# Kernel tuning notes

Hardware: AMD Instinct MI355X
Metric: run time of the kernel (lower is better)

Reference implementation:

```python
import jax, jax.numpy as jnp
import numpy as np

B, T, D_FEAT, FREQ, HID = 256, 128, 128, 16, 128


def setup_inputs() -> dict:
    key = jax.random.key(0)
    ks = jax.random.split(key, 14)
    n = lambda k, s, sc: jax.random.normal(k, s, jnp.float32) * sc
    sx = float(np.sqrt(2.0 / (D_FEAT + HID)))   # xavier-ish for W_*
    sf = float(np.sqrt(2.0 / (D_FEAT + FREQ)))
    sh = float(np.sqrt(1.0 / HID))              # stand-in for orthogonal U_*
    return {
        "input": jax.random.normal(ks[0], (B, D_FEAT * T), jnp.float32),
        "W_i": n(ks[1], (D_FEAT, HID), sx), "U_i": n(ks[2], (HID, HID), sh), "b_i": jnp.zeros((HID,), jnp.float32),
        "W_ste": n(ks[3], (D_FEAT, HID), sx), "U_ste": n(ks[4], (HID, HID), sh), "b_ste": jnp.ones((HID,), jnp.float32),
        "W_fre": n(ks[5], (D_FEAT, FREQ), sf), "U_fre": n(ks[6], (HID, FREQ), sh), "b_fre": jnp.ones((FREQ,), jnp.float32),
        "W_c": n(ks[7], (D_FEAT, HID), sx), "U_c": n(ks[8], (HID, HID), sh), "b_c": jnp.zeros((HID,), jnp.float32),
        "W_o": n(ks[9], (D_FEAT, HID), sx), "U_o": n(ks[10], (HID, HID), sh), "b_o": jnp.zeros((HID,), jnp.float32),
        "U_a": n(ks[11], (FREQ, 1), sh), "b_a": jnp.zeros((HID,), jnp.float32),
        "W_sym": n(ks[12], (HID, 1), sh), "b_sym": jnp.zeros((1,), jnp.float32),
    }


def _hsig(z):  # torch.nn.Hardsigmoid: relu6(x+3)/6
    return jnp.clip(z / 6.0 + 0.5, 0.0, 1.0)


def reference(input, W_i, U_i, b_i, W_ste, U_ste, b_ste, W_fre, U_fre, b_fre,
              W_c, U_c, b_c, W_o, U_o, b_o, U_a, b_a, W_sym, b_sym):
    Bsz = input.shape[0]
    x = input.reshape(Bsz, D_FEAT, -1).transpose(0, 2, 1)  # (B, T, D)
    # hoist the 5 input projections out of the time loop (identical math)
    xi = jnp.einsum('btd,dh->tbh', x, W_i) + b_i
    xste = jnp.einsum('btd,dh->tbh', x, W_ste) + b_ste
    xfre = jnp.einsum('btd,df->tbf', x, W_fre) + b_fre
    xc = jnp.einsum('btd,dh->tbh', x, W_c) + b_c
    xo = jnp.einsum('btd,dh->tbh', x, W_o) + b_o
    frequency = jnp.arange(FREQ, dtype=jnp.float32) / FREQ
    two_pi = jnp.float32(2.0 * np.pi)
    ua = U_a[:, 0]  # (FREQ,)

    def step(carry, xs):
        h, S_re, S_im, t = carry
        xi_t, xste_t, xfre_t, xc_t, xo_t = xs
        i = _hsig(xi_t + h @ U_i)
        ste = _hsig(xste_t + h @ U_ste)
        fre = _hsig(xfre_t + h @ U_fre)
        f = ste[:, :, None] * fre[:, None, :]          # (B, H, F)
        c = i * jnp.tanh(xc_t + h @ U_c)               # (B, H)
        t = t + 1.0
        omega = two_pi * t * frequency                 # (F,)
        S_re = f * S_re + c[:, :, None] * jnp.cos(omega)
        S_im = f * S_im + c[:, :, None] * jnp.sin(omega)
        A = S_re * S_re + S_im * S_im                  # (B, H, F)
        a = jnp.tanh(jnp.einsum('bhf,f->bh', A, ua) + b_a)
        o = _hsig(xo_t + h @ U_o)
        h = o * a
        return (h, S_re, S_im, t), None

    init = (jnp.zeros((Bsz, HID), jnp.float32),
            jnp.zeros((Bsz, HID, FREQ), jnp.float32),
            jnp.zeros((Bsz, HID, FREQ), jnp.float32),
            jnp.float32(0.0))
    (h, _, _, _), _ = jax.lax.scan(step, init, (xi, xste, xfre, xc, xo))
    return h @ W_sym + b_sym  # (B, num_symbols)
```

## Files before the change

### kernel.cpp

```cpp
#include <hip/hip_runtime.h>
#include <hip/hip_bf16.h>


__device__ __forceinline__ float hsig_f(float z) {
    return fminf(fmaxf(z * (1.0f / 6.0f) + 0.5f, 0.0f), 1.0f);
}

__global__ __launch_bounds__(256, 2) void proj_gemm(
    const float* __restrict__ input,
    const float* __restrict__ Wi, const float* __restrict__ Wste,
    const float* __restrict__ Wc, const float* __restrict__ Wo,
    const float* __restrict__ Wfre,
    const float* __restrict__ bi, const float* __restrict__ bste,
    const float* __restrict__ bc, const float* __restrict__ bo,
    const float* __restrict__ bfre,
    float* __restrict__ P)
{
    __shared__ __align__(16) float XT[128 * 128];
    __shared__ __align__(16) float WT[128 * 128];

    const int b   = blockIdx.x;
    const int tid = threadIdx.x;

    const float* xb = input + (size_t)b * 16384;
#pragma unroll
    for (int i = 0; i < 16; i++) {
        int idx4 = (i * 256 + tid) * 4;
        *(float4*)(&XT[idx4]) = *(const float4*)(xb + idx4);
    }

    const int tx = tid & 15, ty = tid >> 4;
    const int c0 = tx * 8, t0 = ty * 8;

    const float* Ws[5]     = {Wi, Wste, Wc, Wo, Wfre};
    const float* biases[5] = {bi, bste, bc, bo, bfre};

    for (int ct = 0; ct < 5; ct++) {
        const float* W = Ws[ct];
        if (ct < 4) {
#pragma unroll
            for (int i = 0; i < 16; i++) {
                int idx4 = (i * 256 + tid) * 4;
                *(float4*)(&WT[idx4]) = *(const float4*)(W + idx4);
            }
        } else {
#pragma unroll
            for (int i = 0; i < 2; i++) {
                int idx4 = (i * 256 + tid) * 4;
                int d = idx4 >> 4, cc = idx4 & 15;
                *(float4*)(&WT[d * 128 + cc]) = *(const float4*)(W + idx4);
            }
        }
        __syncthreads();

        float acc[8][8] = {};
#pragma unroll 2
        for (int k = 0; k < 128; k++) {
            float4 x0 = *(const float4*)(&XT[k * 128 + t0]);
            float4 x1 = *(const float4*)(&XT[k * 128 + t0 + 4]);
            float4 w0 = *(const float4*)(&WT[k * 128 + c0]);
            float4 w1 = *(const float4*)(&WT[k * 128 + c0 + 4]);
            const float xr[8] = {x0.x, x0.y, x0.z, x0.w, x1.x, x1.y, x1.z, x1.w};
            const float wc[8] = {w0.x, w0.y, w0.z, w0.w, w1.x, w1.y, w1.z, w1.w};
#pragma unroll
            for (int r = 0; r < 8; r++)
#pragma unroll
                for (int cc = 0; cc < 8; cc++)
                    acc[r][cc] = fmaf(xr[r], wc[cc], acc[r][cc]);
        }

        const int  cbase = (ct < 4) ? ct * 128 : 512;
        const bool valid = (ct < 4) || (c0 < 16);
        if (valid) {
            const float* bias = biases[ct];
            float4 b40, b41;
            b40.x = bias[c0 + 0]; b40.y = bias[c0 + 1];
            b40.z = bias[c0 + 2]; b40.w = bias[c0 + 3];
            b41.x = bias[c0 + 4]; b41.y = bias[c0 + 5];
            b41.z = bias[c0 + 6]; b41.w = bias[c0 + 7];
#pragma unroll
            for (int r = 0; r < 8; r++) {
                int row = b * 128 + t0 + r;
                float4 o0, o1;
                o0.x = acc[r][0] + b40.x; o0.y = acc[r][1] + b40.y;
                o0.z = acc[r][2] + b40.z; o0.w = acc[r][3] + b40.w;
                o1.x = acc[r][4] + b41.x; o1.y = acc[r][5] + b41.y;
                o1.z = acc[r][6] + b41.z; o1.w = acc[r][7] + b41.w;
                *(float4*)(&P[(size_t)row * 528 + cbase + c0])     = o0;
                *(float4*)(&P[(size_t)row * 528 + cbase + c0 + 4]) = o1;
            }
        }
        __syncthreads();
    }
}

__global__ __launch_bounds__(1024, 4) void recur_kernel(
    const float* __restrict__ P,
    const float* __restrict__ Ui, const float* __restrict__ Uste,
    const float* __restrict__ Uc, const float* __restrict__ Uo,
    const float* __restrict__ Ufre,
    const float* __restrict__ Ua, const float* __restrict__ ba_g,
    const float* __restrict__ Wsym, const float* __restrict__ bsym,
    float* __restrict__ out)
{
    __shared__ float ufre_t[16 * 132];
    __shared__ float costab[16], sintab[16];
    __shared__ float gate_buf[512];
    __shared__ float partial_buf[512];
    __shared__ float fre_buf[16];
    __shared__ float h_buf[128];

    const int tid  = threadIdx.x;
    const int lane = tid & 63;
    const int half = tid >> 9;
    const int c    = tid & 511;
    const int m    = c >> 7;
    const int j    = c & 127;
    const int hh   = tid >> 3;
    const int fsel = tid & 7;
    const int b    = blockIdx.x;

    for (int e = tid; e < 2048; e += 1024) {
        int k = e >> 4, col = e & 15;
        ufre_t[col * 132 + k] = Ufre[e];
    }
    if (tid < 16) {
        float ang = 6.283185307179586f * (float)tid * (1.0f / 16.0f);
        costab[tid] = cosf(ang);
        sintab[tid] = sinf(ang);
    }
    if (tid < 128) h_buf[tid] = 0.0f;

    const float* Uptr = (m == 0) ? Ui : (m == 1) ? Uste : (m == 2) ? Uc : Uo;
    const volatile float* Uv = (const volatile float*)Uptr;
    float Ucol[64];
#pragma unroll
    for (int k = 0; k < 64; k++) Ucol[k] = Uv[(half * 64 + k) * 128 + j];

    const float ua0 = Ua[fsel];
    const float ua1 = Ua[fsel + 8];
    const float ba  = ba_g[hh];

    float hA = 0.0f;
    float Sre0 = 0.f, Sim0 = 0.f, Sre1 = 0.f, Sim1 = 0.f;
    int idx0 = 0, idx1 = 0;

    __syncthreads();

    const float* pr = P + (size_t)b * 128 * 528;
    for (int t = 0; t < 128; t++) {
        const float xpre = (half == 0) ? pr[c] : pr[512 + (c >> 5)];

        float a0 = 0.f, a1 = 0.f;
#pragma unroll
        for (int kk = 0; kk < 64; kk += 2) {
            float s0 = __uint_as_float(__builtin_amdgcn_readlane(__float_as_uint(hA), kk));
            float s1 = __uint_as_float(__builtin_amdgcn_readlane(__float_as_uint(hA), kk + 1));
            a0 = fmaf(s0, Ucol[kk],     a0);
            a1 = fmaf(s1, Ucol[kk + 1], a1);
        }
        float acc = a0 + a1;

        if (half) partial_buf[c] = acc;
        __syncthreads();

        if (half == 0) {
            float z = acc + partial_buf[c] + xpre;
            float g = (m == 2) ? tanhf(z) : hsig_f(z);
            gate_buf[c] = g;
        } else {
            const int col = c >> 5, kg = c & 31;
            float4 hv = *(const float4*)(&h_buf[kg * 4]);
            float4 uv = *(const float4*)(&ufre_t[col * 132 + kg * 4]);
            float p = fmaf(hv.x, uv.x, fmaf(hv.y, uv.y, fmaf(hv.z, uv.z, hv.w * uv.w)));
#pragma unroll
            for (int off = 1; off <= 16; off <<= 1) p += __shfl_xor(p, off, 64);
            if (kg == 0) fre_buf[col] = hsig_f(p + xpre);
        }
        __syncthreads();

        {
            float iv = gate_buf[hh];
            float sv = gate_buf[128 + hh];
            float tc = gate_buf[256 + hh];
            float ov = gate_buf[384 + hh];
            float cg = iv * tc;

            idx0 = (idx0 + fsel) & 15;
            idx1 = (idx1 + fsel + 8) & 15;

            float f0v = sv * fre_buf[fsel];
            float f1v = sv * fre_buf[fsel + 8];
            Sre0 = fmaf(f0v, Sre0, cg * costab[idx0]);
            Sim0 = fmaf(f0v, Sim0, cg * sintab[idx0]);
            Sre1 = fmaf(f1v, Sre1, cg * costab[idx1]);
            Sim1 = fmaf(f1v, Sim1, cg * sintab[idx1]);

            float aacc = fmaf(Sre0, Sre0, Sim0 * Sim0) * ua0;
            aacc = fmaf(fmaf(Sre1, Sre1, Sim1 * Sim1), ua1, aacc);
            aacc += __shfl_xor(aacc, 1, 64);
            aacc += __shfl_xor(aacc, 2, 64);
            aacc += __shfl_xor(aacc, 4, 64);
            if (fsel == 0) {
                float a = tanhf(aacc + ba);
                h_buf[hh] = ov * a;
            }
        }
        __syncthreads();
        hA = h_buf[half * 64 + lane];
        pr += 528;
    }

    if (tid < 64) {
        float v = fmaf(h_buf[lane], Wsym[lane], h_buf[64 + lane] * Wsym[64 + lane]);
#pragma unroll
        for (int off = 1; off <= 32; off <<= 1) v += __shfl_xor(v, off, 64);
        if (lane == 0) out[b] = v + bsym[0];
    }
}

extern "C" void kernel_launch(void* const* d_in, const int* in_sizes, int n_in,
                              void* d_out, int out_size, void* d_ws, size_t ws_size,
                              hipStream_t stream) {
    const float* input = (const float*)d_in[0];
    const float* W_i   = (const float*)d_in[1];
    const float* U_i   = (const float*)d_in[2];
    const float* b_i   = (const float*)d_in[3];
    const float* W_ste = (const float*)d_in[4];
    const float* U_ste = (const float*)d_in[5];
    const float* b_ste = (const float*)d_in[6];
    const float* W_fre = (const float*)d_in[7];
    const float* U_fre = (const float*)d_in[8];
    const float* b_fre = (const float*)d_in[9];
    const float* W_c   = (const float*)d_in[10];
    const float* U_c   = (const float*)d_in[11];
    const float* b_c   = (const float*)d_in[12];
    const float* W_o   = (const float*)d_in[13];
    const float* U_o   = (const float*)d_in[14];
    const float* b_o   = (const float*)d_in[15];
    const float* U_a   = (const float*)d_in[16];
    const float* b_a   = (const float*)d_in[17];
    const float* W_sym = (const float*)d_in[18];
    const float* b_sym = (const float*)d_in[19];

    float* P = (float*)d_ws;

    proj_gemm<<<256, 256, 0, stream>>>(
        input, W_i, W_ste, W_c, W_o, W_fre,
        b_i, b_ste, b_c, b_o, b_fre, P);

    recur_kernel<<<256, 1024, 0, stream>>>(
        P, U_i, U_ste, U_c, U_o, U_fre,
        U_a, b_a, W_sym, b_sym, (float*)d_out);
}
```

Before: 434.2 us.

## Split projection GEMM over time halves and pin recurrence kernel occupancy attributes

The projection GEMM now launches two blocks per batch element, each covering 64 timesteps, with smaller shared tiles (XT 128x64, WT padded to 66 columns) processed in 64-column passes with an 8x2 register tile. This doubles grid parallelism and cuts LDS per block so more blocks can be resident, at the cost of more W reloads and less register reuse per FMA. The recurrence kernel swaps launch_bounds for explicit amdgpu flat-work-group-size and waves-per-eu attributes, and adds a compiler memory barrier after the U column preload to pin register allocation and scheduling.

Result: faster. 412.4 us (-5.0%).

```diff
diff --git a/kernel.cpp b/kernel.cpp
--- a/kernel.cpp
+++ b/kernel.cpp
@@ -6,7 +6,7 @@
     return fminf(fmaxf(z * (1.0f / 6.0f) + 0.5f, 0.0f), 1.0f);
 }
 
-__global__ __launch_bounds__(256, 2) void proj_gemm(
+__global__ __launch_bounds__(256) void proj_gemm(
     const float* __restrict__ input,
     const float* __restrict__ Wi, const float* __restrict__ Wste,
     const float* __restrict__ Wc, const float* __restrict__ Wo,
@@ -16,85 +16,79 @@
     const float* __restrict__ bfre,
     float* __restrict__ P)
 {
-    __shared__ __align__(16) float XT[128 * 128];
-    __shared__ __align__(16) float WT[128 * 128];
-
-    const int b   = blockIdx.x;
+    __shared__ __align__(16) float XT[128 * 64];
+    __shared__ __align__(16) float WT[128 * 66];
+
+    const int br  = blockIdx.x;
+    const int b   = br >> 1;
+    const int t0g = (br & 1) * 64;
     const int tid = threadIdx.x;
 
-    const float* xb = input + (size_t)b * 16384;
-#pragma unroll
-    for (int i = 0; i < 16; i++) {
-        int idx4 = (i * 256 + tid) * 4;
-        *(float4*)(&XT[idx4]) = *(const float4*)(xb + idx4);
-    }
-
-    const int tx = tid & 15, ty = tid >> 4;
-    const int c0 = tx * 8, t0 = ty * 8;
+    const float* xb = input + (size_t)b * 16384 + t0g;
+#pragma unroll
+    for (int i = 0; i < 8; i++) {
+        int f = (i * 256 + tid) * 4;
+        int k = f >> 6, t = f & 63;
+        *(float4*)(&XT[k * 64 + t]) = *(const float4*)(xb + k * 128 + t);
+    }
+
+    const int tx = tid & 31;
+    const int ty = tid >> 5;
 
     const float* Ws[5]     = {Wi, Wste, Wc, Wo, Wfre};
     const float* biases[5] = {bi, bste, bc, bo, bfre};
 
     for (int ct = 0; ct < 5; ct++) {
-        const float* W = Ws[ct];
-        if (ct < 4) {
-#pragma unroll
-            for (int i = 0; i < 16; i++) {
-                int idx4 = (i * 256 + tid) * 4;
-                *(float4*)(&WT[idx4]) = *(const float4*)(W + idx4);
-            }
-        } else {
-#pragma unroll
-            for (int i = 0; i < 2; i++) {
-                int idx4 = (i * 256 + tid) * 4;
-                int d = idx4 >> 4, cc = idx4 & 15;
-                *(float4*)(&WT[d * 128 + cc]) = *(const float4*)(W + idx4);
-            }
-        }
-        __syncthreads();
-
-        float acc[8][8] = {};
-#pragma unroll 2
-        for (int k = 0; k < 128; k++) {
-            float4 x0 = *(const float4*)(&XT[k * 128 + t0]);
-            float4 x1 = *(const float4*)(&XT[k * 128 + t0 + 4]);
-            float4 w0 = *(const float4*)(&WT[k * 128 + c0]);
-            float4 w1 = *(const float4*)(&WT[k * 128 + c0 + 4]);
-            const float xr[8] = {x0.x, x0.y, x0.z, x0.w, x1.x, x1.y, x1.z, x1.w};
-            const float wc[8] = {w0.x, w0.y, w0.z, w0.w, w1.x, w1.y, w1.z, w1.w};
-#pragma unroll
-            for (int r = 0; r < 8; r++)
-#pragma unroll
-                for (int cc = 0; cc < 8; cc++)
-                    acc[r][cc] = fmaf(xr[r], wc[cc], acc[r][cc]);
-        }
-
-        const int  cbase = (ct < 4) ? ct * 128 : 512;
-        const bool valid = (ct < 4) || (c0 < 16);
-        if (valid) {
-            const float* bias = biases[ct];
-            float4 b40, b41;
-            b40.x = bias[c0 + 0]; b40.y = bias[c0 + 1];
-            b40.z = bias[c0 + 2]; b40.w = bias[c0 + 3];
-            b41.x = bias[c0 + 4]; b41.y = bias[c0 + 5];
-            b41.z = bias[c0 + 6]; b41.w = bias[c0 + 7];
-#pragma unroll
-            for (int r = 0; r < 8; r++) {
-                int row = b * 128 + t0 + r;
-                float4 o0, o1;
-                o0.x = acc[r][0] + b40.x; o0.y = acc[r][1] + b40.y;
-                o0.z = acc[r][2] + b40.z; o0.w = acc[r][3] + b40.w;
-                o1.x = acc[r][4] + b41.x; o1.y = acc[r][5] + b41.y;
-                o1.z = acc[r][6] + b41.z; o1.w = acc[r][7] + b41.w;
-                *(float4*)(&P[(size_t)row * 528 + cbase + c0])     = o0;
-                *(float4*)(&P[(size_t)row * 528 + cbase + c0 + 4]) = o1;
-            }
-        }
-        __syncthreads();
-    }
-}
-
-__global__ __launch_bounds__(1024, 4) void recur_kernel(
+        const float* W     = Ws[ct];
+        const float* bias  = biases[ct];
+        const int    ncols = (ct < 4) ? 128 : 16;
+        const int    npass = (ct < 4) ? 2 : 1;
+        const int    cbase = (ct < 4) ? ct * 128 : 512;
+
+        for (int ch = 0; ch < npass; ch++) {
+            __syncthreads();
+#pragma unroll
+            for (int i = 0; i < 8; i++) {
+                int f = (i * 256 + tid) * 4;
+                int k = f >> 6, c = f & 63;
+                int gc = ch * 64 + c;
+                if (gc < ncols)
+                    *(float4*)(&WT[k * 66 + c]) = *(const float4*)(W + k * ncols + gc);
+            }
+            __syncthreads();
+
+            float acc[8][2] = {};
+#pragma unroll 4
+            for (int k = 0; k < 128; k++) {
+                float2 w  = *(const float2*)(&WT[k * 66 + tx * 2]);
+                float4 x0 = *(const float4*)(&XT[k * 64 + ty * 8]);
+                float4 x1 = *(const float4*)(&XT[k * 64 + ty * 8 + 4]);
+                const float xr[8] = {x0.x, x0.y, x0.z, x0.w, x1.x, x1.y, x1.z, x1.w};
+#pragma unroll
+                for (int r = 0; r < 8; r++) {
+                    acc[r][0] = fmaf(xr[r], w.x, acc[r][0]);
+                    acc[r][1] = fmaf(xr[r], w.y, acc[r][1]);
+                }
+            }
+
+            const int colg = ch * 64 + tx * 2;
+            if (colg < ncols) {
+                float b0 = bias[colg], b1 = bias[colg + 1];
+#pragma unroll
+                for (int r = 0; r < 8; r++) {
+                    int row = br * 64 + ty * 8 + r;
+                    float2 o = make_float2(acc[r][0] + b0, acc[r][1] + b1);
+                    *(float2*)(&P[(size_t)row * 528 + cbase + colg]) = o;
+                }
+            }
+        }
+    }
+}
+
+__global__
+__attribute__((amdgpu_flat_work_group_size(1024, 1024)))
+__attribute__((amdgpu_waves_per_eu(4, 4)))
+void recur_kernel(
     const float* __restrict__ P,
     const float* __restrict__ Ui, const float* __restrict__ Uste,
     const float* __restrict__ Uc, const float* __restrict__ Uo,
@@ -136,6 +130,7 @@
     float Ucol[64];
 #pragma unroll
     for (int k = 0; k < 64; k++) Ucol[k] = Uv[(half * 64 + k) * 128 + j];
+    asm volatile("" ::: "memory");
 
     const float ua0 = Ua[fsel];
     const float ua1 = Ua[fsel + 8];
@@ -245,7 +240,7 @@
 
     float* P = (float*)d_ws;
 
-    proj_gemm<<<256, 256, 0, stream>>>(
+    proj_gemm<<<512, 256, 0, stream>>>(
         input, W_i, W_ste, W_c, W_o, W_fre,
         b_i, b_ste, b_c, b_o, b_fre, P);
 
```
